# Performance work log

Measured on AMD Instinct MI355X. Metric: run time of the kernel, lower is better.

The kernel has to match this reference:

```python
import jax, jax.numpy as jnp
import numpy as np

BATCH, NATOMS, NBONDS, NSPEC = 50, 512, 4096, 2


def _taper(r, rmin, rmax):
    # taper() from the source (bond-order cutoff smoothing)
    r3 = jnp.where(r > rmax, 1.0, 0.0)
    ok = (r <= rmax) & (r > rmin)
    r2 = jnp.where(ok, r, 0.0)
    r20 = jnp.where(ok, 1.0, 0.0)
    rterm = 1.0 / (rmin - rmax) ** 3
    rm = rmin * r20
    rd = rm - r2
    trm1 = rm + 2.0 * r2 - 3.0 * rmax * r20
    return rterm * rd * rd * trm1 + r3


def _fnn(xs, wi, w, b, wo, bo):
    # tiny sigmoid MLP fnn(): xs [B,NB,3] -> [B,NB]
    o = jax.nn.sigmoid(xs @ wi)              # [B,NB,8]
    for l in range(w.shape[0]):
        o = jax.nn.sigmoid(o @ w[l] + b[l])  # [B,NB,8]
    return jax.nn.sigmoid(o @ wo + bo)[..., 0]


def _forward(x, cell, rcell, sp_p, gp, bp, fe_wi, fe_w, fe_b, fe_wo, fe_bo, bdid, spec):
    lp1, ovun3, ovun4, ovun6, ovun7, ovun8, botol = (gp[i] for i in range(7))
    rosi, ropi, ropp, bo1, bo2, bo3, bo4, bo5, bo6, Desi = (bp[i] for i in range(10))
    B, N = x.shape[0], x.shape[1]
    # fvr + minimum image: vr[b,i,j] = x[b,i] - x[b,j]
    vr = x[:, :, None, :] - x[:, None, :, :]          # [B,N,N,3]
    vrf = jnp.einsum('bijk,bkl->bijl', vr, rcell)
    vrf = jnp.where(vrf > 0.5, vrf - 1.0, vrf)
    vrf = jnp.where(vrf < -0.5, vrf + 1.0, vrf)
    vr = jnp.einsum('bijk,bkl->bijl', vrf, cell)
    r = jnp.sqrt(jnp.sum(vr * vr, axis=3))            # [B,N,N]

    i0, i1 = bdid[:, 0], bdid[:, 1]
    rbd = r[:, i0, i1]                                # gather bonded pairs [B,NB]
    # uncorrected bond orders (get_bondorder_uc)
    eterm1 = (1.0 + botol) * jnp.exp(bo1 * (rbd / rosi) ** bo2)
    eterm2 = jnp.exp(bo3 * (rbd / ropi) ** bo4)
    eterm3 = jnp.exp(bo5 * (rbd / ropp) ** bo6)
    bop_si_v = _taper(eterm1, botol, 2.0 * botol) * (eterm1 - botol)
    bop_pi_v = _taper(eterm2, botol, 2.0 * botol) * eterm2
    bop_pp_v = _taper(eterm3, botol, 2.0 * botol) * eterm3

    def sym(v):  # symmetric scatter into dense [B,N,N]
        z = jnp.zeros((B, N, N), v.dtype)
        return z.at[:, i0, i1].set(v).at[:, i1, i0].set(v)

    bop_si = sym(bop_si_v)
    bop_pi = sym(bop_pi_v)
    bop_pp = sym(bop_pp_v)
    bop = bop_si + bop_pi + bop_pp
    Delta = jnp.sum(bop, axis=2)                      # [B,N]
    Delta_pi = jnp.sum(bop_pi + bop_pp, axis=2)
    SO = jnp.sum(bop_si, axis=2)

    # bond energy: fnn on (bosi,bopi,bopp), ebond = sum over scattered ebd matrix
    xs = jnp.stack([bop_si_v, bop_pi_v, bop_pp_v], axis=2)  # [B,NB,3]
    esi = _fnn(xs, fe_wi, fe_w, fe_b, fe_wo, fe_bo)
    ebond = jnp.sum(-Desi * esi, axis=1)              # [B]

    # per-species gather of atomic params (vectorized species loop)
    pa = sp_p[spec]                                   # [N,5]
    val, vale, lp2, ovun2, ovun5 = pa[:, 0], pa[:, 1], pa[:, 2], pa[:, 3], pa[:, 4]

    # get_elone
    Nlp = 0.5 * (vale - val)
    delta_e = 0.5 * (Delta - vale)
    De = -jax.nn.relu(-jnp.ceil(delta_e))
    nlp = -De + jnp.exp(-lp1 * 4.0 * jnp.square(1.0 + delta_e - De))
    Delta_lp = jax.nn.relu(Nlp - nlp + 1.0) - 1.0
    Elone = lp2 * Delta_lp / (1.0 + jnp.exp(-75.0 * Delta_lp))

    # get_eover
    dlpcorr = Delta - val - Delta_lp / (1.0 + ovun3 * jnp.exp(ovun4 * Delta_pi))
    denom = dlpcorr + val
    otrm1 = 1.0 / jnp.where(denom != 0.0, denom, 1e-8)  # DIV_IF
    Eover = SO * otrm1 * dlpcorr * jax.nn.sigmoid(-ovun2 * dlpcorr)

    # get_eunder
    Eunder = (-ovun5 * (1.0 - jnp.exp(ovun6 * dlpcorr)) * jax.nn.sigmoid(ovun2 * dlpcorr)
              / (1.0 + ovun7 * jnp.exp(ovun8 * Delta_pi)))

    return ebond + jnp.sum(Elone + Eover + Eunder, axis=1)  # total energy per frame [B]


def setup_inputs() -> dict:
    key = jax.random.key(0)
    ks = jax.random.split(key, 8)
    L = 20.0  # cubic cell edge (Angstrom)
    x = jax.random.uniform(ks[0], (BATCH, NATOMS, 3), dtype=jnp.float32) * L
    cell = jnp.tile(jnp.eye(3, dtype=jnp.float32) * L, (BATCH, 1, 1))
    rcell = jnp.tile(jnp.eye(3, dtype=jnp.float32) / L, (BATCH, 1, 1))
    rng = np.random.default_rng(0)
    i0 = rng.integers(0, NATOMS, NBONDS)
    j0 = (i0 + rng.integers(1, NATOMS, NBONDS)) % NATOMS
    bdid = jnp.asarray(np.stack([np.minimum(i0, j0), np.maximum(i0, j0)], 1), dtype=jnp.int32)
    spec = jax.random.randint(ks[1], (NATOMS,), 0, NSPEC, dtype=jnp.int32)
    # [val, vale, lp2, ovun2, ovun5] per species
    sp_p = jnp.array([[4.0, 4.0, 0.1, -4.0, 30.0],
                      [2.0, 6.0, 15.0, -4.0, 30.0]], jnp.float32)
    # [lp1, ovun3, ovun4, ovun6, ovun7, ovun8, botol]
    gp = jnp.array([18.0, 3.0, 5.0, 8.0, 11.0, 13.0, 0.01], jnp.float32)
    # [rosi, ropi, ropp, bo1, bo2, bo3, bo4, bo5, bo6, Desi]
    bp = jnp.array([1.4, 1.2, 1.1, -0.08, 6.0, -0.1, 7.0, -0.2, 8.0, 120.0], jnp.float32)
    fe_wi = jax.random.normal(ks[2], (3, 8), jnp.float32)
    fe_w = jax.random.normal(ks[3], (5, 8, 8), jnp.float32) * 0.5
    fe_b = jax.random.normal(ks[4], (5, 8), jnp.float32) * 0.1
    fe_wo = jax.random.normal(ks[5], (8, 1), jnp.float32)
    fe_bo = jax.random.normal(ks[6], (1,), jnp.float32) * 0.1
    return dict(x=x, cell=cell, rcell=rcell, sp_p=sp_p, gp=gp, bp=bp,
                fe_wi=fe_wi, fe_w=fe_w, fe_b=fe_b, fe_wo=fe_wo, fe_bo=fe_bo,
                bdid=bdid, spec=spec)


def reference(x, cell, rcell, sp_p, gp, bp, fe_wi, fe_w, fe_b, fe_wo, fe_bo, bdid, spec):
    return _forward(x, cell, rcell, sp_p, gp, bp, fe_wi, fe_w, fe_b, fe_wo, fe_bo, bdid, spec)
```

## Files before the change

### kernel.cpp

```cpp
#include <hip/hip_runtime.h>

#define BATCH 50
#define NATOMS 512
#define NBONDS 4096
#define NXF (NATOMS*3)
#define ILP 2
#define BPB (NBONDS/(256*ILP))
#define BITS_W (NATOMS*NATOMS/32)

__device__ __forceinline__ float sigmoidf_(float x){ return 1.f/(1.f+__expf(-x)); }

__device__ __forceinline__ float taperf_(float r, float rmin, float rmax){
    float r3  = (r > rmax) ? 1.f : 0.f;
    bool  ok  = (r <= rmax) && (r > rmin);
    float r2  = ok ? r   : 0.f;
    float r20 = ok ? 1.f : 0.f;
    float d   = rmin - rmax;
    float rterm = 1.f/(d*d*d);
    float rm  = rmin*r20;
    float rd  = rm - r2;
    float trm1 = rm + 2.f*r2 - 3.f*rmax*r20;
    return rterm*rd*rd*trm1 + r3;
}

__global__ __launch_bounds__(1024) void claim_kernel(const int* __restrict__ bdid,
                                                     float* __restrict__ ownerf,
                                                     unsigned* __restrict__ done){
    __shared__ unsigned bits[BITS_W];
    int tid = threadIdx.x;
    for(int t=tid; t<BITS_W; t+=1024) bits[t] = 0u;
    if(tid < BATCH) done[tid] = 0u;
    __syncthreads();
    for(int k=tid; k<NBONDS; k+=1024){
        int2 ij = ((const int2*)bdid)[k];
        unsigned pidx = (unsigned)(ij.x*NATOMS + ij.y);
        unsigned old = atomicOr(&bits[pidx>>5], 1u<<(pidx&31));
        ownerf[k] = ((old>>(pidx&31)) & 1u) ? 0.f : 1.f;
    }
}

__global__ __launch_bounds__(256) void fused_kernel(
    const float* __restrict__ x, const float* __restrict__ cell, const float* __restrict__ rcell,
    const float* __restrict__ sp_p, const float* __restrict__ gp, const float* __restrict__ bp,
    const float* __restrict__ fe_wi, const float* __restrict__ fe_w, const float* __restrict__ fe_b,
    const float* __restrict__ fe_wo, const float* __restrict__ fe_bo,
    const int* __restrict__ bdid, const int* __restrict__ spec,
    const float* __restrict__ ownerf,
    float* __restrict__ Dpart, float* __restrict__ Ppart, float* __restrict__ Spart,
    float* __restrict__ epart, unsigned* __restrict__ done,
    float* __restrict__ out)
{
    __shared__ float s_x[NXF];
    __shared__ float accD[NATOMS], accP[NATOMS], accS[NATOMS];
    __shared__ __align__(16) float s_w[320];
    __shared__ __align__(16) float s_wo[8];
    __shared__ float s_wi[24], s_bb[40];
    __shared__ float s_part[4];
    __shared__ unsigned s_rank;
    int tid = threadIdx.x;
    int b   = blockIdx.y;

    const float4* xb4 = (const float4*)(x + (size_t)b*NXF);
    float4* sx4 = (float4*)s_x;
    sx4[tid] = xb4[tid];
    if(tid < NXF/4 - 256) sx4[tid+256] = xb4[tid+256];
    for(int n=tid; n<NATOMS; n+=256){ accD[n]=0.f; accP[n]=0.f; accS[n]=0.f; }
    for(int t=tid; t<320; t+=256){
        int l = t>>6, rr = t&63, v = rr>>3, u = rr&7;
        s_w[(l<<6) + (u<<3) + v] = fe_w[t];
    }
    if(tid < 24) s_wi[tid] = fe_wi[tid];
    if(tid < 40) s_bb[tid] = fe_b[tid];
    if(tid < 8)  s_wo[tid] = fe_wo[tid];
    __syncthreads();

    float botol = gp[6];
    float rosi=bp[0], ropi=bp[1], ropp=bp[2];
    float bo1=bp[3], bo2=bp[4], bo3=bp[5], bo4=bp[6], bo5=bp[7], bo6=bp[8], Desi=bp[9];
    float bo_out = fe_bo[0];
    const float* cb = cell  + b*9;
    const float* rb = rcell + b*9;
    float tmax = 2.f*botol;

    int kbase = blockIdx.x*(256*ILP) + tid;
    float o[ILP][8];

    #pragma unroll
    for(int q=0;q<ILP;q++){
        int k = kbase + q*256;
        float own = ownerf[k];
        int2 ij = ((const int2*)bdid)[k];
        int i = ij.x, j = ij.y;
        float dx0 = s_x[3*i+0]-s_x[3*j+0];
        float dx1 = s_x[3*i+1]-s_x[3*j+1];
        float dx2 = s_x[3*i+2]-s_x[3*j+2];
        float f0 = dx0*rb[0]+dx1*rb[3]+dx2*rb[6];
        float f1 = dx0*rb[1]+dx1*rb[4]+dx2*rb[7];
        float f2 = dx0*rb[2]+dx1*rb[5]+dx2*rb[8];
        f0 = (f0>0.5f)?f0-1.f:f0; f0 = (f0<-0.5f)?f0+1.f:f0;
        f1 = (f1>0.5f)?f1-1.f:f1; f1 = (f1<-0.5f)?f1+1.f:f1;
        f2 = (f2>0.5f)?f2-1.f:f2; f2 = (f2<-0.5f)?f2+1.f:f2;
        float v0 = f0*cb[0]+f1*cb[3]+f2*cb[6];
        float v1 = f0*cb[1]+f1*cb[4]+f2*cb[7];
        float v2 = f0*cb[2]+f1*cb[5]+f2*cb[8];
        float r = sqrtf(v0*v0+v1*v1+v2*v2);

        float eterm1 = (1.f+botol)*__expf(bo1*__powf(r/rosi, bo2));
        float eterm2 = __expf(bo3*__powf(r/ropi, bo4));
        float eterm3 = __expf(bo5*__powf(r/ropp, bo6));
        float si = taperf_(eterm1, botol, tmax)*(eterm1-botol);
        float pi = taperf_(eterm2, botol, tmax)*eterm2;
        float pp = taperf_(eterm3, botol, tmax)*eterm3;

        float bop = own*(si+pi+pp), dpi = own*(pi+pp), osi = own*si;
        atomicAdd(&accD[i], bop); atomicAdd(&accD[j], bop);
        atomicAdd(&accP[i], dpi); atomicAdd(&accP[j], dpi);
        atomicAdd(&accS[i], osi); atomicAdd(&accS[j], osi);

        #pragma unroll
        for(int u=0;u<8;u++)
            o[q][u] = sigmoidf_(si*s_wi[u] + pi*s_wi[8+u] + pp*s_wi[16+u]);
    }

    #pragma unroll
    for(int l=0;l<5;l++){
        const float4* wl = (const float4*)(s_w + (l<<6));
        const float*  bl = s_bb + (l<<3);
        float no[ILP][8];
        #pragma unroll
        for(int u=0;u<8;u++){
            float4 wa = wl[2*u], wb = wl[2*u+1];
            #pragma unroll
            for(int q=0;q<ILP;q++){
                float a0 = fmaf(o[q][0],wa.x, bl[u]);
                float a1 = o[q][1]*wa.y;
                a0 = fmaf(o[q][2],wa.z,a0); a1 = fmaf(o[q][3],wa.w,a1);
                a0 = fmaf(o[q][4],wb.x,a0); a1 = fmaf(o[q][5],wb.y,a1);
                a0 = fmaf(o[q][6],wb.z,a0); a1 = fmaf(o[q][7],wb.w,a1);
                no[q][u] = sigmoidf_(a0+a1);
            }
        }
        #pragma unroll
        for(int q=0;q<ILP;q++)
            #pragma unroll
            for(int u=0;u<8;u++) o[q][u]=no[q][u];
    }
    float4 woa = ((const float4*)s_wo)[0], wob = ((const float4*)s_wo)[1];
    float esum = 0.f;
    #pragma unroll
    for(int q=0;q<ILP;q++){
        float a0 = fmaf(o[q][0],woa.x, bo_out);
        float a1 = o[q][1]*woa.y;
        a0 = fmaf(o[q][2],woa.z,a0); a1 = fmaf(o[q][3],woa.w,a1);
        a0 = fmaf(o[q][4],wob.x,a0); a1 = fmaf(o[q][5],wob.y,a1);
        a0 = fmaf(o[q][6],wob.z,a0); a1 = fmaf(o[q][7],wob.w,a1);
        esum += sigmoidf_(a0+a1);
    }

    float ev = -Desi*esum;
    #pragma unroll
    for(int o2=32;o2>0;o2>>=1) ev += __shfl_down(ev, o2, 64);
    if((tid & 63) == 0) s_part[tid>>6] = ev;
    __syncthreads();

    size_t sl = ((size_t)b*BPB + blockIdx.x)*NATOMS;
    for(int n=tid; n<NATOMS; n+=256){
        __hip_atomic_store(&Dpart[sl+n], accD[n], __ATOMIC_RELAXED, __HIP_MEMORY_SCOPE_AGENT);
        __hip_atomic_store(&Ppart[sl+n], accP[n], __ATOMIC_RELAXED, __HIP_MEMORY_SCOPE_AGENT);
        __hip_atomic_store(&Spart[sl+n], accS[n], __ATOMIC_RELAXED, __HIP_MEMORY_SCOPE_AGENT);
    }
    if(tid==0)
        __hip_atomic_store(&epart[b*BPB + blockIdx.x],
                           s_part[0]+s_part[1]+s_part[2]+s_part[3],
                           __ATOMIC_RELAXED, __HIP_MEMORY_SCOPE_AGENT);

    __syncthreads();
    if(tid==0) s_rank = atomicAdd(&done[b], 1u);
    __syncthreads();
    if(s_rank != BPB-1) return;

    float lp1=gp[0], ovun3=gp[1], ovun4=gp[2], ovun6=gp[3], ovun7=gp[4], ovun8=gp[5];
    float acc = 0.f;
    for(int n=tid; n<NATOMS; n+=256){
        float D=0.f, Dpi=0.f, so=0.f;
        size_t base = (size_t)b*BPB*NATOMS + n;
        #pragma unroll
        for(int blk=0; blk<BPB; blk++){
            size_t idx = base + (size_t)blk*NATOMS;
            D   += __hip_atomic_load(&Dpart[idx], __ATOMIC_RELAXED, __HIP_MEMORY_SCOPE_AGENT);
            Dpi += __hip_atomic_load(&Ppart[idx], __ATOMIC_RELAXED, __HIP_MEMORY_SCOPE_AGENT);
            so  += __hip_atomic_load(&Spart[idx], __ATOMIC_RELAXED, __HIP_MEMORY_SCOPE_AGENT);
        }
        int s = spec[n];
        const float* pa = sp_p + s*5;
        float val=pa[0], vale=pa[1], lp2=pa[2], ovun2=pa[3], ovun5=pa[4];

        float Nlp = 0.5f*(vale-val);
        float de  = 0.5f*(D-vale);
        float De  = fminf(ceilf(de), 0.f);
        float t   = 1.f + de - De;
        float nlp = -De + __expf(-lp1*4.f*t*t);
        float Dlp = fmaxf(Nlp - nlp + 1.f, 0.f) - 1.f;
        float Elone = lp2*Dlp/(1.f+__expf(-75.f*Dlp));
        float dlp = D - val - Dlp/(1.f + ovun3*__expf(ovun4*Dpi));
        float denom = dlp + val;
        float otrm1 = 1.f/((denom!=0.f)?denom:1e-8f);
        float Eover = so*otrm1*dlp*sigmoidf_(-ovun2*dlp);
        float Eunder = -ovun5*(1.f-__expf(ovun6*dlp))*sigmoidf_(ovun2*dlp)
                       /(1.f + ovun7*__expf(ovun8*Dpi));
        acc += Elone + Eover + Eunder;
    }
    #pragma unroll
    for(int o2=32;o2>0;o2>>=1) acc += __shfl_down(acc, o2, 64);
    __syncthreads();
    if((tid & 63) == 0) s_part[tid>>6] = acc;
    __syncthreads();
    if(tid==0){
        float eb = 0.f;
        #pragma unroll
        for(int blk=0; blk<BPB; blk++)
            eb += __hip_atomic_load(&epart[b*BPB + blk], __ATOMIC_RELAXED, __HIP_MEMORY_SCOPE_AGENT);
        out[b] = eb + s_part[0]+s_part[1]+s_part[2]+s_part[3];
    }
}

extern "C" void kernel_launch(void* const* d_in, const int* in_sizes, int n_in,
                              void* d_out, int out_size, void* d_ws, size_t ws_size,
                              hipStream_t stream)
{
    const float* x     = (const float*)d_in[0];
    const float* cell  = (const float*)d_in[1];
    const float* rcell = (const float*)d_in[2];
    const float* sp_p  = (const float*)d_in[3];
    const float* gp    = (const float*)d_in[4];
    const float* bp    = (const float*)d_in[5];
    const float* fe_wi = (const float*)d_in[6];
    const float* fe_w  = (const float*)d_in[7];
    const float* fe_b  = (const float*)d_in[8];
    const float* fe_wo = (const float*)d_in[9];
    const float* fe_bo = (const float*)d_in[10];
    const int*   bdid  = (const int*)d_in[11];
    const int*   spec  = (const int*)d_in[12];
    float* out = (float*)d_out;

    float* Dpart  = (float*)d_ws;
    float* Ppart  = Dpart + (size_t)BATCH*BPB*NATOMS;
    float* Spart  = Ppart + (size_t)BATCH*BPB*NATOMS;
    float* epart  = Spart + (size_t)BATCH*BPB*NATOMS;
    unsigned* done = (unsigned*)(epart + BATCH*BPB);
    float* ownerf  = (float*)(done + BATCH);

    claim_kernel<<<dim3(1), 1024, 0, stream>>>(bdid, ownerf, done);
    fused_kernel<<<dim3(BPB, BATCH), 256, 0, stream>>>(
        x, cell, rcell, sp_p, gp, bp, fe_wi, fe_w, fe_b, fe_wo, fe_bo,
        bdid, spec, ownerf, Dpart, Ppart, Spart, epart, done, out);
}
```

Before: 110.9 us.

## Split fused last-block reduction into separate bond and atom kernels

Replaces the atomic done-counter with last-block-finishes pattern by a third kernel launch that reduces per-block partials and computes per-atom energies with one thread per atom. This removes atomic stores and loads, the counter reset and the tail serialization in the last block per batch. In exchange it adds a kernel launch and a round trip of the partial arrays through global memory.

Result: faster. 108.1 us (-2.5%).

```diff
diff --git a/kernel.cpp b/kernel.cpp
--- a/kernel.cpp
+++ b/kernel.cpp
@@ -24,12 +24,10 @@
 }
 
 __global__ __launch_bounds__(1024) void claim_kernel(const int* __restrict__ bdid,
-                                                     float* __restrict__ ownerf,
-                                                     unsigned* __restrict__ done){
+                                                     float* __restrict__ ownerf){
     __shared__ unsigned bits[BITS_W];
     int tid = threadIdx.x;
     for(int t=tid; t<BITS_W; t+=1024) bits[t] = 0u;
-    if(tid < BATCH) done[tid] = 0u;
     __syncthreads();
     for(int k=tid; k<NBONDS; k+=1024){
         int2 ij = ((const int2*)bdid)[k];
@@ -39,16 +37,14 @@
     }
 }
 
-__global__ __launch_bounds__(256) void fused_kernel(
+__global__ __launch_bounds__(256) void bond_kernel(
     const float* __restrict__ x, const float* __restrict__ cell, const float* __restrict__ rcell,
-    const float* __restrict__ sp_p, const float* __restrict__ gp, const float* __restrict__ bp,
+    const float* __restrict__ gp, const float* __restrict__ bp,
     const float* __restrict__ fe_wi, const float* __restrict__ fe_w, const float* __restrict__ fe_b,
     const float* __restrict__ fe_wo, const float* __restrict__ fe_bo,
-    const int* __restrict__ bdid, const int* __restrict__ spec,
-    const float* __restrict__ ownerf,
+    const int* __restrict__ bdid, const float* __restrict__ ownerf,
     float* __restrict__ Dpart, float* __restrict__ Ppart, float* __restrict__ Spart,
-    float* __restrict__ epart, unsigned* __restrict__ done,
-    float* __restrict__ out)
+    float* __restrict__ epart)
 {
     __shared__ float s_x[NXF];
     __shared__ float accD[NATOMS], accP[NATOMS], accS[NATOMS];
@@ -56,7 +52,6 @@
     __shared__ __align__(16) float s_wo[8];
     __shared__ float s_wi[24], s_bb[40];
     __shared__ float s_part[4];
-    __shared__ unsigned s_rank;
     int tid = threadIdx.x;
     int b   = blockIdx.y;
 
@@ -165,62 +160,64 @@
 
     size_t sl = ((size_t)b*BPB + blockIdx.x)*NATOMS;
     for(int n=tid; n<NATOMS; n+=256){
-        __hip_atomic_store(&Dpart[sl+n], accD[n], __ATOMIC_RELAXED, __HIP_MEMORY_SCOPE_AGENT);
-        __hip_atomic_store(&Ppart[sl+n], accP[n], __ATOMIC_RELAXED, __HIP_MEMORY_SCOPE_AGENT);
-        __hip_atomic_store(&Spart[sl+n], accS[n], __ATOMIC_RELAXED, __HIP_MEMORY_SCOPE_AGENT);
-    }
-    if(tid==0)
-        __hip_atomic_store(&epart[b*BPB + blockIdx.x],
-                           s_part[0]+s_part[1]+s_part[2]+s_part[3],
-                           __ATOMIC_RELAXED, __HIP_MEMORY_SCOPE_AGENT);
-
-    __syncthreads();
-    if(tid==0) s_rank = atomicAdd(&done[b], 1u);
-    __syncthreads();
-    if(s_rank != BPB-1) return;
-
+        Dpart[sl+n] = accD[n];
+        Ppart[sl+n] = accP[n];
+        Spart[sl+n] = accS[n];
+    }
+    if(tid==0) epart[b*BPB + blockIdx.x] = s_part[0]+s_part[1]+s_part[2]+s_part[3];
+}
+
+__global__ __launch_bounds__(512) void atom_kernel(
+    const float* __restrict__ sp_p, const float* __restrict__ gp,
+    const int* __restrict__ spec,
+    const float* __restrict__ Dpart, const float* __restrict__ Ppart,
+    const float* __restrict__ Spart, const float* __restrict__ epart,
+    float* __restrict__ out)
+{
+    __shared__ float s_red[8];
+    int tid = threadIdx.x;
+    int b   = blockIdx.x;
     float lp1=gp[0], ovun3=gp[1], ovun4=gp[2], ovun6=gp[3], ovun7=gp[4], ovun8=gp[5];
-    float acc = 0.f;
-    for(int n=tid; n<NATOMS; n+=256){
-        float D=0.f, Dpi=0.f, so=0.f;
-        size_t base = (size_t)b*BPB*NATOMS + n;
-        #pragma unroll
-        for(int blk=0; blk<BPB; blk++){
-            size_t idx = base + (size_t)blk*NATOMS;
-            D   += __hip_atomic_load(&Dpart[idx], __ATOMIC_RELAXED, __HIP_MEMORY_SCOPE_AGENT);
-            Dpi += __hip_atomic_load(&Ppart[idx], __ATOMIC_RELAXED, __HIP_MEMORY_SCOPE_AGENT);
-            so  += __hip_atomic_load(&Spart[idx], __ATOMIC_RELAXED, __HIP_MEMORY_SCOPE_AGENT);
-        }
-        int s = spec[n];
-        const float* pa = sp_p + s*5;
-        float val=pa[0], vale=pa[1], lp2=pa[2], ovun2=pa[3], ovun5=pa[4];
-
-        float Nlp = 0.5f*(vale-val);
-        float de  = 0.5f*(D-vale);
-        float De  = fminf(ceilf(de), 0.f);
-        float t   = 1.f + de - De;
-        float nlp = -De + __expf(-lp1*4.f*t*t);
-        float Dlp = fmaxf(Nlp - nlp + 1.f, 0.f) - 1.f;
-        float Elone = lp2*Dlp/(1.f+__expf(-75.f*Dlp));
-        float dlp = D - val - Dlp/(1.f + ovun3*__expf(ovun4*Dpi));
-        float denom = dlp + val;
-        float otrm1 = 1.f/((denom!=0.f)?denom:1e-8f);
-        float Eover = so*otrm1*dlp*sigmoidf_(-ovun2*dlp);
-        float Eunder = -ovun5*(1.f-__expf(ovun6*dlp))*sigmoidf_(ovun2*dlp)
-                       /(1.f + ovun7*__expf(ovun8*Dpi));
-        acc += Elone + Eover + Eunder;
-    }
+
+    float D=0.f, Dpi=0.f, so=0.f;
+    size_t base = (size_t)b*BPB*NATOMS + tid;
+    #pragma unroll
+    for(int blk=0; blk<BPB; blk++){
+        size_t idx = base + (size_t)blk*NATOMS;
+        D   += Dpart[idx];
+        Dpi += Ppart[idx];
+        so  += Spart[idx];
+    }
+    int s = spec[tid];
+    const float* pa = sp_p + s*5;
+    float val=pa[0], vale=pa[1], lp2=pa[2], ovun2=pa[3], ovun5=pa[4];
+
+    float Nlp = 0.5f*(vale-val);
+    float de  = 0.5f*(D-vale);
+    float De  = fminf(ceilf(de), 0.f);
+    float t   = 1.f + de - De;
+    float nlp = -De + __expf(-lp1*4.f*t*t);
+    float Dlp = fmaxf(Nlp - nlp + 1.f, 0.f) - 1.f;
+    float Elone = lp2*Dlp/(1.f+__expf(-75.f*Dlp));
+    float dlp = D - val - Dlp/(1.f + ovun3*__expf(ovun4*Dpi));
+    float denom = dlp + val;
+    float otrm1 = 1.f/((denom!=0.f)?denom:1e-8f);
+    float Eover = so*otrm1*dlp*sigmoidf_(-ovun2*dlp);
+    float Eunder = -ovun5*(1.f-__expf(ovun6*dlp))*sigmoidf_(ovun2*dlp)
+                   /(1.f + ovun7*__expf(ovun8*Dpi));
+    float acc = Elone + Eover + Eunder;
+
     #pragma unroll
     for(int o2=32;o2>0;o2>>=1) acc += __shfl_down(acc, o2, 64);
-    __syncthreads();
-    if((tid & 63) == 0) s_part[tid>>6] = acc;
+    if((tid & 63) == 0) s_red[tid>>6] = acc;
     __syncthreads();
     if(tid==0){
-        float eb = 0.f;
-        #pragma unroll
-        for(int blk=0; blk<BPB; blk++)
-            eb += __hip_atomic_load(&epart[b*BPB + blk], __ATOMIC_RELAXED, __HIP_MEMORY_SCOPE_AGENT);
-        out[b] = eb + s_part[0]+s_part[1]+s_part[2]+s_part[3];
+        float tot = 0.f;
+        #pragma unroll
+        for(int w=0;w<8;w++) tot += s_red[w];
+        #pragma unroll
+        for(int blk=0; blk<BPB; blk++) tot += epart[b*BPB + blk];
+        out[b] = tot;
     }
 }
 
@@ -247,11 +244,12 @@
     float* Ppart  = Dpart + (size_t)BATCH*BPB*NATOMS;
     float* Spart  = Ppart + (size_t)BATCH*BPB*NATOMS;
     float* epart  = Spart + (size_t)BATCH*BPB*NATOMS;
-    unsigned* done = (unsigned*)(epart + BATCH*BPB);
-    float* ownerf  = (float*)(done + BATCH);
-
-    claim_kernel<<<dim3(1), 1024, 0, stream>>>(bdid, ownerf, done);
-    fused_kernel<<<dim3(BPB, BATCH), 256, 0, stream>>>(
-        x, cell, rcell, sp_p, gp, bp, fe_wi, fe_w, fe_b, fe_wo, fe_bo,
-        bdid, spec, ownerf, Dpart, Ppart, Spart, epart, done, out);
-}
+    float* ownerf = epart + BATCH*BPB;
+
+    claim_kernel<<<dim3(1), 1024, 0, stream>>>(bdid, ownerf);
+    bond_kernel<<<dim3(BPB, BATCH), 256, 0, stream>>>(
+        x, cell, rcell, gp, bp, fe_wi, fe_w, fe_b, fe_wo, fe_bo,
+        bdid, ownerf, Dpart, Ppart, Spart, epart);
+    atom_kernel<<<dim3(BATCH), 512, 0, stream>>>(
+        sp_p, gp, spec, Dpart, Ppart, Spart, epart, out);
+}
```
